# Kernel tuning notes

Hardware: AMD Instinct MI355X
Metric: run time of the kernel (lower is better)

Reference implementation:

```python
import jax, jax.numpy as jnp
import numpy as np

H = 1024      # hidden_size
V = 50257     # output_size (vocab)
L = 512       # max_length (encoder length)


def setup_inputs() -> dict:
    key = jax.random.key(0)
    ks = jax.random.split(key, 12)
    s = 0.02  # param init scale
    return {
        "input": jax.random.randint(ks[0], (1, 1), 0, V),
        "hidden": jax.random.normal(ks[1], (1, 1, H), dtype=jnp.float32),
        "encoder_outputs": jax.random.normal(ks[2], (L, H), dtype=jnp.float32),
        "emb": jax.random.normal(ks[3], (V, H), dtype=jnp.float32) * s,
        "attn_W": jax.random.normal(ks[4], (L, 2 * H), dtype=jnp.float32) * s,
        "attn_b": jnp.zeros((L,), jnp.float32),
        "comb_W": jax.random.normal(ks[5], (H, 2 * H), dtype=jnp.float32) * s,
        "comb_b": jnp.zeros((H,), jnp.float32),
        "W_ih": jax.random.normal(ks[6], (4 * H, H), dtype=jnp.float32) * s,
        "W_hh": jax.random.normal(ks[7], (4 * H, H), dtype=jnp.float32) * s,
        "b_ih": jnp.zeros((4 * H,), jnp.float32),
        "b_hh": jnp.zeros((4 * H,), jnp.float32),
        "out_W": jax.random.normal(ks[8], (V, H), dtype=jnp.float32) * s,
        "out_b": jnp.zeros((V,), jnp.float32),
    }


def reference(input, hidden, encoder_outputs, emb, attn_W, attn_b,
              comb_W, comb_b, W_ih, W_hh, b_ih, b_hh, out_W, out_b):
    # embedding lookup -> [1, H] (embedded[0] in the torch code)
    embedded = emb[input.reshape(-1)].reshape(1, H)
    h0 = hidden[0]  # [1, H]
    # Bahdanau-style attention over encoder positions
    attn_logits = jnp.concatenate([embedded, h0], axis=1) @ attn_W.T + attn_b  # [1, L]
    attn_weights = jax.nn.softmax(attn_logits, axis=1)
    attn_applied = attn_weights @ encoder_outputs  # [1, H]
    # combine + relu
    x = jax.nn.relu(jnp.concatenate([embedded, attn_applied], axis=1) @ comb_W.T + comb_b)  # [1, H]
    # single LSTM cell step; torch passes (hidden, hidden) so c0 == h0
    c0 = h0
    gates = x @ W_ih.T + b_ih + h0 @ W_hh.T + b_hh  # [1, 4H], gate order i,f,g,o
    i_g, f_g, g_g, o_g = jnp.split(gates, 4, axis=1)
    c = jax.nn.sigmoid(f_g) * c0 + jax.nn.sigmoid(i_g) * jnp.tanh(g_g)
    h = jax.nn.sigmoid(o_g) * jnp.tanh(c)
    # output projection + log-softmax
    out = jax.nn.log_softmax(h @ out_W.T + out_b, axis=1)  # [1, V]
    return out, (h[None], c[None]), attn_weights
```

## Files before the change

### kernel.cpp

```cpp
#include <hip/hip_runtime.h>
#include <math.h>

#define H 1024
#define V 50257
#define L 512

#define WS_ATTN  0
#define WS_DEN   1024
#define WS_E     1088
#define WS_X     1600
#define WS_H     2624
#define WS_VLOG  3648
#define WS_PART  53905
#define MEMSET_BYTES 4096

__device__ __forceinline__ float wave_sum(float v) {
    for (int o = 32; o > 0; o >>= 1) v += __shfl_down(v, o, 64);
    return v;
}
__device__ __forceinline__ float sigf(float x) { return 1.0f / (1.0f + expf(-x)); }
__device__ __forceinline__ float dot4(float4 a, float4 b) {
    return a.x * b.x + a.y * b.y + a.z * b.z + a.w * b.w;
}

__global__ __launch_bounds__(256) void kAB(const int* __restrict__ tok,
                                           const float* __restrict__ hidden,
                                           const float* __restrict__ enc,
                                           const float* __restrict__ emb,
                                           const float* __restrict__ attn_W,
                                           const float* __restrict__ attn_b,
                                           float* __restrict__ ws) {
    const int bid = blockIdx.x, t = threadIdx.x;
    const int w = t >> 6, l = t & 63;
    const int jb = bid >> 6, c = bid & 63;
    const size_t token = (size_t)tok[0];
    const float4* ev4 = (const float4*)(emb + token * H);
    const float4* hv4 = (const float4*)hidden;

    __shared__ float esh[8];

    {
        int r0 = c * 8 + w * 2;
        int r1 = r0 + 1;
        const float4* rw0 = (const float4*)(attn_W + (size_t)r0 * 2 * H);
        const float4* rw1 = (const float4*)(attn_W + (size_t)r1 * 2 * H);
        float a0 = 0.f, a1 = 0.f;
#pragma unroll
        for (int i = 0; i < 4; ++i) {
            float4 e4 = ev4[i * 64 + l], h4 = hv4[i * 64 + l];
            a0 += dot4(rw0[i * 64 + l], e4) + dot4(rw0[256 + i * 64 + l], h4);
            a1 += dot4(rw1[i * 64 + l], e4) + dot4(rw1[256 + i * 64 + l], h4);
        }
        float s0 = wave_sum(a0);
        float s1 = wave_sum(a1);
        if (l == 0) {
            esh[w * 2]     = expf(s0 + attn_b[r0]);
            esh[w * 2 + 1] = expf(s1 + attn_b[r1]);
        }
    }
    __syncthreads();
    if (jb == 0) {
        if (t < 8) ws[WS_E + c * 8 + t] = esh[t];
        if (t == 0) {
            float p = 0.f;
#pragma unroll
            for (int i = 0; i < 8; ++i) p += esh[i];
            ws[WS_DEN + c] = p;
        }
    }
    int j = jb * 256 + t;
    float acc = 0.f;
#pragma unroll
    for (int i = 0; i < 8; ++i)
        acc += esh[i] * enc[(size_t)(c * 8 + i) * H + j];
    atomicAdd(&ws[WS_ATTN + j], acc);
}

__global__ __launch_bounds__(256) void kC_combine(const int* __restrict__ tok,
                                                  const float* __restrict__ emb,
                                                  const float* __restrict__ comb_W,
                                                  const float* __restrict__ comb_b,
                                                  float* __restrict__ ws,
                                                  float* __restrict__ out) {
    const int bid = blockIdx.x, t = threadIdx.x;
    const int w = t >> 6, l = t & 63;
    __shared__ float Ssh;
    float dv = (t < 64) ? ws[WS_DEN + t] : 0.f;
    if (w == 0) {
        float s = wave_sum(dv);
        if (t == 0) Ssh = s;
    }
    __syncthreads();
    float invS = 1.0f / Ssh;

    if (bid < 2) out[V + 2 * H + bid * 256 + t] = ws[WS_E + bid * 256 + t] * invS;

    const size_t token = (size_t)tok[0];
    const float4* ev4 = (const float4*)(emb + token * H);
    const float4* a4 = (const float4*)(ws + WS_ATTN);
    int r = bid * 4 + w;
    const float4* cw = (const float4*)comb_W;
    float aL = 0.f, aR = 0.f;
#pragma unroll
    for (int i = 0; i < 4; ++i) {
        aL += dot4(cw[(size_t)r * 512 + i * 64 + l], ev4[i * 64 + l]);
        aR += dot4(cw[(size_t)r * 512 + 256 + i * 64 + l], a4[i * 64 + l]);
    }
    float s = wave_sum(aL + aR * invS);
    if (l == 0) ws[WS_X + r] = fmaxf(s + comb_b[r], 0.0f);
}

__global__ __launch_bounds__(256) void kD_gates_lstm(const float* __restrict__ hidden,
                                                     const float* __restrict__ W_ih,
                                                     const float* __restrict__ W_hh,
                                                     const float* __restrict__ b_ih,
                                                     const float* __restrict__ b_hh,
                                                     float* __restrict__ ws,
                                                     float* __restrict__ out) {
    const int n = blockIdx.x, t = threadIdx.x;
    const int w = t >> 6, l = t & 63;
    __shared__ float4 xs[256], hs[256];
    __shared__ float gsh[4];
    xs[t] = ((const float4*)(ws + WS_X))[t];
    hs[t] = ((const float4*)hidden)[t];
    __syncthreads();
    int row = w * H + n;
    const float4* wi = (const float4*)W_ih;
    const float4* wh = (const float4*)W_hh;
    float acc = 0.f;
#pragma unroll
    for (int i = 0; i < 4; ++i) {
        acc += dot4(wi[(size_t)row * 256 + i * 64 + l], xs[i * 64 + l]);
        acc += dot4(wh[(size_t)row * 256 + i * 64 + l], hs[i * 64 + l]);
    }
    float s = wave_sum(acc);
    if (l == 0) gsh[w] = s + b_ih[row] + b_hh[row];
    __syncthreads();
    if (t == 0) {
        float c0 = hidden[n];
        float cc = sigf(gsh[1]) * c0 + sigf(gsh[0]) * tanhf(gsh[2]);
        float hh = sigf(gsh[3]) * tanhf(cc);
        ws[WS_H + n] = hh;
        out[V + n] = hh;
        out[V + H + n] = cc;
    }
}

__global__ __launch_bounds__(256) void kE_vocab(const float* __restrict__ out_W,
                                                const float* __restrict__ out_b,
                                                float* __restrict__ ws) {
    const int bid = blockIdx.x, t = threadIdx.x;
    const int w = t >> 6, l = t & 63;
    const int row0 = bid * 24 + (bid < 1105 ? bid : 1105);
    const int cnt  = 24 + (bid < 1105 ? 1 : 0);

    const float4* h4 = (const float4*)(ws + WS_H);
    float4 hr[4];
#pragma unroll
    for (int i = 0; i < 4; ++i) hr[i] = h4[i * 64 + l];

    const float4* ow = (const float4*)out_W;
    float es = 0.f;
    int wq = (cnt + 3) >> 2;
    int kb = w * wq;
    int ke = kb + wq < cnt ? kb + wq : cnt;
    for (int k = kb; k < ke; k += 2) {
        bool has1 = (k + 1 < ke);
        int k1 = has1 ? k + 1 : k;
        int r0 = row0 + k, r1 = row0 + k1;
        const float4* q0 = ow + (size_t)r0 * 256;
        const float4* q1 = ow + (size_t)r1 * 256;
        float a0 = 0.f, a1 = 0.f;
#pragma unroll
        for (int i = 0; i < 4; ++i) {
            a0 += dot4(q0[i * 64 + l], hr[i]);
            a1 += dot4(q1[i * 64 + l], hr[i]);
        }
        float s0 = wave_sum(a0);
        float s1 = wave_sum(a1);
        if (l == 0) {
            float lg0 = s0 + out_b[r0];
            ws[WS_VLOG + r0] = lg0;
            es += expf(lg0);
            if (has1) {
                float lg1 = s1 + out_b[r1];
                ws[WS_VLOG + r1] = lg1;
                es += expf(lg1);
            }
        }
    }
    __shared__ float red[4];
    if (l == 0) red[w] = es;
    __syncthreads();
    if (t == 0) ws[WS_PART + bid] = red[0] + red[1] + red[2] + red[3];
}

__global__ __launch_bounds__(256) void kF_logsoftmax(const float* __restrict__ ws,
                                                     float* __restrict__ out) {
    const int bid = blockIdx.x, t = threadIdx.x;
    float ps = 0.f;
#pragma unroll
    for (int k = 0; k < 8; ++k) ps += ws[WS_PART + k * 256 + t];
    float s = wave_sum(ps);
    __shared__ float red[4];
    __shared__ float lsh;
    if ((t & 63) == 0) red[t >> 6] = s;
    __syncthreads();
    if (t == 0) lsh = logf(red[0] + red[1] + red[2] + red[3]);
    __syncthreads();
    float lse = lsh;
    const int row0 = bid * 196 + (bid < 81 ? bid : 81);
    const int cnt  = 196 + (bid < 81 ? 1 : 0);
    for (int i = t; i < cnt; i += 256)
        out[row0 + i] = ws[WS_VLOG + row0 + i] - lse;
}

extern "C" void kernel_launch(void* const* d_in, const int* in_sizes, int n_in,
                              void* d_out, int out_size, void* d_ws, size_t ws_size,
                              hipStream_t stream) {
    const int*   tok     = (const int*)d_in[0];
    const float* hidden  = (const float*)d_in[1];
    const float* enc     = (const float*)d_in[2];
    const float* emb     = (const float*)d_in[3];
    const float* attn_W  = (const float*)d_in[4];
    const float* attn_b  = (const float*)d_in[5];
    const float* comb_W  = (const float*)d_in[6];
    const float* comb_b  = (const float*)d_in[7];
    const float* W_ih    = (const float*)d_in[8];
    const float* W_hh    = (const float*)d_in[9];
    const float* b_ih    = (const float*)d_in[10];
    const float* b_hh    = (const float*)d_in[11];
    const float* out_W   = (const float*)d_in[12];
    const float* out_b   = (const float*)d_in[13];
    float* out = (float*)d_out;
    float* ws  = (float*)d_ws;

    hipMemsetAsync(ws, 0, MEMSET_BYTES, stream);
    kAB<<<256, 256, 0, stream>>>(tok, hidden, enc, emb, attn_W, attn_b, ws);
    kC_combine<<<256, 256, 0, stream>>>(tok, emb, comb_W, comb_b, ws, out);
    kD_gates_lstm<<<1024, 256, 0, stream>>>(hidden, W_ih, W_hh, b_ih, b_hh, ws, out);
    kE_vocab<<<2048, 256, 0, stream>>>(out_W, out_b, ws);
    kF_logsoftmax<<<256, 256, 0, stream>>>(ws, out);
}
```

Baseline: 60.20 us.

## Repartition attention kernel, add nontemporal weight loads, interleave vocab row assignment

The attention kernel now runs 512-thread blocks covering 128 chunks of 4 encoder rows, with 512 output columns each, so each block does less logit work and writes wider. The combine kernel reduces the 128 partial denominators across two waves, and the workspace offsets shift to make room for them. Weight matrix reads in the attention, combine and gate kernels switch to nontemporal loads to avoid polluting the cache with single-use data. The vocab kernel assigns rows to waves in an interleaved pattern instead of contiguous chunks, which may help coalescing across waves but changes the DRAM access pattern.

```diff
diff --git a/kernel.cpp b/kernel.cpp
--- a/kernel.cpp
+++ b/kernel.cpp
@@ -7,12 +7,14 @@
 
 #define WS_ATTN  0
 #define WS_DEN   1024
-#define WS_E     1088
-#define WS_X     1600
-#define WS_H     2624
-#define WS_VLOG  3648
-#define WS_PART  53905
+#define WS_E     1152
+#define WS_X     1664
+#define WS_H     2688
+#define WS_VLOG  3712
+#define WS_PART  53969
 #define MEMSET_BYTES 4096
+
+typedef float vfloat4 __attribute__((ext_vector_type(4)));
 
 __device__ __forceinline__ float wave_sum(float v) {
     for (int o = 32; o > 0; o >>= 1) v += __shfl_down(v, o, 64);
@@ -22,8 +24,12 @@
 __device__ __forceinline__ float dot4(float4 a, float4 b) {
     return a.x * b.x + a.y * b.y + a.z * b.z + a.w * b.w;
 }
-
-__global__ __launch_bounds__(256) void kAB(const int* __restrict__ tok,
+__device__ __forceinline__ float4 ntload4(const float4* p) {
+    vfloat4 v = __builtin_nontemporal_load((const vfloat4*)p);
+    return make_float4(v.x, v.y, v.z, v.w);
+}
+
+__global__ __launch_bounds__(512) void kAB(const int* __restrict__ tok,
                                            const float* __restrict__ hidden,
                                            const float* __restrict__ enc,
                                            const float* __restrict__ emb,
@@ -32,47 +38,35 @@
                                            float* __restrict__ ws) {
     const int bid = blockIdx.x, t = threadIdx.x;
     const int w = t >> 6, l = t & 63;
-    const int jb = bid >> 6, c = bid & 63;
+    const int jb = bid >> 7, c = bid & 127;
     const size_t token = (size_t)tok[0];
     const float4* ev4 = (const float4*)(emb + token * H);
     const float4* hv4 = (const float4*)hidden;
 
-    __shared__ float esh[8];
-
-    {
-        int r0 = c * 8 + w * 2;
-        int r1 = r0 + 1;
-        const float4* rw0 = (const float4*)(attn_W + (size_t)r0 * 2 * H);
-        const float4* rw1 = (const float4*)(attn_W + (size_t)r1 * 2 * H);
-        float a0 = 0.f, a1 = 0.f;
+    __shared__ float esh[4];
+
+    if (w < 4) {
+        int r = c * 4 + w;
+        const float4* rw = (const float4*)(attn_W + (size_t)r * 2 * H);
+        float a = 0.f;
 #pragma unroll
         for (int i = 0; i < 4; ++i) {
-            float4 e4 = ev4[i * 64 + l], h4 = hv4[i * 64 + l];
-            a0 += dot4(rw0[i * 64 + l], e4) + dot4(rw0[256 + i * 64 + l], h4);
-            a1 += dot4(rw1[i * 64 + l], e4) + dot4(rw1[256 + i * 64 + l], h4);
+            a += dot4(ntload4(&rw[i * 64 + l]), ev4[i * 64 + l]);
+            a += dot4(ntload4(&rw[256 + i * 64 + l]), hv4[i * 64 + l]);
         }
-        float s0 = wave_sum(a0);
-        float s1 = wave_sum(a1);
-        if (l == 0) {
-            esh[w * 2]     = expf(s0 + attn_b[r0]);
-            esh[w * 2 + 1] = expf(s1 + attn_b[r1]);
-        }
+        float s = wave_sum(a);
+        if (l == 0) esh[w] = expf(s + attn_b[r]);
     }
     __syncthreads();
     if (jb == 0) {
-        if (t < 8) ws[WS_E + c * 8 + t] = esh[t];
-        if (t == 0) {
-            float p = 0.f;
-#pragma unroll
-            for (int i = 0; i < 8; ++i) p += esh[i];
-            ws[WS_DEN + c] = p;
-        }
-    }
-    int j = jb * 256 + t;
+        if (t < 4) ws[WS_E + c * 4 + t] = esh[t];
+        if (t == 0) ws[WS_DEN + c] = esh[0] + esh[1] + esh[2] + esh[3];
+    }
+    int j = jb * 512 + t;
     float acc = 0.f;
 #pragma unroll
-    for (int i = 0; i < 8; ++i)
-        acc += esh[i] * enc[(size_t)(c * 8 + i) * H + j];
+    for (int i = 0; i < 4; ++i)
+        acc += esh[i] * enc[(size_t)(c * 4 + i) * H + j];
     atomicAdd(&ws[WS_ATTN + j], acc);
 }
 
@@ -84,14 +78,14 @@
                                                   float* __restrict__ out) {
     const int bid = blockIdx.x, t = threadIdx.x;
     const int w = t >> 6, l = t & 63;
-    __shared__ float Ssh;
-    float dv = (t < 64) ? ws[WS_DEN + t] : 0.f;
-    if (w == 0) {
+    __shared__ float red2[2];
+    float dv = (t < 128) ? ws[WS_DEN + t] : 0.f;
+    if (w < 2) {
         float s = wave_sum(dv);
-        if (t == 0) Ssh = s;
-    }
-    __syncthreads();
-    float invS = 1.0f / Ssh;
+        if (l == 0) red2[w] = s;
+    }
+    __syncthreads();
+    float invS = 1.0f / (red2[0] + red2[1]);
 
     if (bid < 2) out[V + 2 * H + bid * 256 + t] = ws[WS_E + bid * 256 + t] * invS;
 
@@ -103,8 +97,8 @@
     float aL = 0.f, aR = 0.f;
 #pragma unroll
     for (int i = 0; i < 4; ++i) {
-        aL += dot4(cw[(size_t)r * 512 + i * 64 + l], ev4[i * 64 + l]);
-        aR += dot4(cw[(size_t)r * 512 + 256 + i * 64 + l], a4[i * 64 + l]);
+        aL += dot4(ntload4(&cw[(size_t)r * 512 + i * 64 + l]), ev4[i * 64 + l]);
+        aR += dot4(ntload4(&cw[(size_t)r * 512 + 256 + i * 64 + l]), a4[i * 64 + l]);
     }
     float s = wave_sum(aL + aR * invS);
     if (l == 0) ws[WS_X + r] = fmaxf(s + comb_b[r], 0.0f);
@@ -130,8 +124,8 @@
     float acc = 0.f;
 #pragma unroll
     for (int i = 0; i < 4; ++i) {
-        acc += dot4(wi[(size_t)row * 256 + i * 64 + l], xs[i * 64 + l]);
-        acc += dot4(wh[(size_t)row * 256 + i * 64 + l], hs[i * 64 + l]);
+        acc += dot4(ntload4(&wi[(size_t)row * 256 + i * 64 + l]), xs[i * 64 + l]);
+        acc += dot4(ntload4(&wh[(size_t)row * 256 + i * 64 + l]), hs[i * 64 + l]);
     }
     float s = wave_sum(acc);
     if (l == 0) gsh[w] = s + b_ih[row] + b_hh[row];
@@ -161,13 +155,10 @@
 
     const float4* ow = (const float4*)out_W;
     float es = 0.f;
-    int wq = (cnt + 3) >> 2;
-    int kb = w * wq;
-    int ke = kb + wq < cnt ? kb + wq : cnt;
-    for (int k = kb; k < ke; k += 2) {
-        bool has1 = (k + 1 < ke);
-        int k1 = has1 ? k + 1 : k;
-        int r0 = row0 + k, r1 = row0 + k1;
+    for (int k = w; k < cnt; k += 8) {
+        int k1 = k + 4;
+        bool has1 = (k1 < cnt);
+        int r0 = row0 + k, r1 = row0 + (has1 ? k1 : k);
         const float4* q0 = ow + (size_t)r0 * 256;
         const float4* q1 = ow + (size_t)r1 * 256;
         float a0 = 0.f, a1 = 0.f;
@@ -235,8 +226,8 @@
     float* out = (float*)d_out;
     float* ws  = (float*)d_ws;
 
-    hipMemsetAsync(ws, 0, MEMSET_BYTES, stream);
-    kAB<<<256, 256, 0, stream>>>(tok, hidden, enc, emb, attn_W, attn_b, ws);
+    (void)hipMemsetAsync(ws, 0, MEMSET_BYTES, stream);
+    kAB<<<256, 512, 0, stream>>>(tok, hidden, enc, emb, attn_W, attn_b, ws);
     kC_combine<<<256, 256, 0, stream>>>(tok, emb, comb_W, comb_b, ws, out);
     kD_gates_lstm<<<1024, 256, 0, stream>>>(hidden, W_ih, W_hh, b_ih, b_hh, ws, out);
     kE_vocab<<<2048, 256, 0, stream>>>(out_W, out_b, ws);
```

New measurement: 61.08 us. Within noise of the previous version (+1.5%).
